# Performance work log

Hardware: AMD Instinct MI355X
Metric: run time of the kernel (lower is better)

## Reference

```python
import jax, jax.numpy as jnp
import numpy as np

C_S, C_Z, C_H = 384, 128, 32
N, L = 4, 384
EPS = 1e-5  # torch LayerNorm default


def setup_inputs() -> dict:
    key = jax.random.key(0)
    ks = jax.random.split(key, 8)
    s = jax.random.normal(ks[0], (N, L, C_S), dtype=jnp.float32)
    ln_g = jnp.ones((C_S,), jnp.float32)
    ln_b = jnp.zeros((C_S,), jnp.float32)
    W1 = jax.random.normal(ks[1], (C_S, C_H), jnp.float32) / np.sqrt(C_S)
    b1 = jax.random.normal(ks[2], (C_H,), jnp.float32) * 0.02
    W2 = jax.random.normal(ks[3], (C_S, C_H), jnp.float32) / np.sqrt(C_S)
    b2 = jax.random.normal(ks[4], (C_H,), jnp.float32) * 0.02
    # linear_out has init='final' (zeros) in training; use random values for a
    # meaningful numerical baseline.
    Wo = jax.random.normal(ks[5], (C_H * C_H, C_Z), jnp.float32) / np.sqrt(C_H * C_H)
    bo = jax.random.normal(ks[6], (C_Z,), jnp.float32) * 0.02
    return {"s": s, "ln_g": ln_g, "ln_b": ln_b, "W1": W1, "b1": b1,
            "W2": W2, "b2": b2, "Wo": Wo, "bo": bo}


def reference(s, ln_g, ln_b, W1, b1, W2, b2, Wo, bo):
    # LayerNorm over c_s
    mu = jnp.mean(s, axis=-1, keepdims=True)
    var = jnp.mean(jnp.square(s - mu), axis=-1, keepdims=True)
    sn = (s - mu) * jax.lax.rsqrt(var + EPS) * ln_g + ln_b
    a = sn @ W1 + b1  # [N, L, c_h]
    b = sn @ W2 + b2  # [N, L, c_h]
    # Original: outer product a[n,i,c]*b[n,j,d] flattened as c*c_h+d, then linear_out.
    # Algebraically fused: never materialize the [N,L,L,c_h^2] tensor.
    Wo3 = Wo.reshape(C_H, C_H, C_Z)  # index order (c, d, z) matches c*c_h+d flattening
    z = jnp.einsum('nic,njd,cdz->nijz', a, b, Wo3, optimize=True) + bo
    return z  # [N, L, L, c_z]
```

## Files before the change

### kernel.cpp

```cpp
#include <hip/hip_runtime.h>
#include <hip/hip_bf16.h>

#define CS 384
#define CH 32
#define CZ 128
#define LL 384
#define NL 1536
#define EPS 1e-5f

typedef float v2f __attribute__((ext_vector_type(2)));
typedef float v4f __attribute__((ext_vector_type(4)));
typedef short s8v __attribute__((ext_vector_type(8)));
typedef unsigned short u8s __attribute__((ext_vector_type(8)));

static __device__ __forceinline__ unsigned short f2bf(float x) {
    unsigned int b = __float_as_uint(x);
    b += 0x7FFFu + ((b >> 16) & 1u);
    return (unsigned short)(b >> 16);
}

__global__ __launch_bounds__(128) void k_ln_ab(
    const float* __restrict__ s, const float* __restrict__ g, const float* __restrict__ be,
    const float* __restrict__ W1, const float* __restrict__ b1,
    const float* __restrict__ W2, const float* __restrict__ b2,
    float* __restrict__ A, float* __restrict__ B)
{
    const int row = blockIdx.x;
    const int t   = threadIdx.x;
    const int wid = t >> 6, lane = t & 63;
    const float* srow = s + (size_t)row * CS;

    __shared__ float sn[CS];
    __shared__ float red[2];
    __shared__ float part[128];

    float x0 = srow[t], x1 = srow[t + 128], x2 = srow[t + 256];

    float p = x0 + x1 + x2;
    #pragma unroll
    for (int o = 32; o > 0; o >>= 1) p += __shfl_down(p, o);
    if (lane == 0) red[wid] = p;
    __syncthreads();
    const float mu = (red[0] + red[1]) * (1.0f / CS);
    __syncthreads();

    float d0 = x0 - mu, d1 = x1 - mu, d2 = x2 - mu;
    float q = d0 * d0 + d1 * d1 + d2 * d2;
    #pragma unroll
    for (int o = 32; o > 0; o >>= 1) q += __shfl_down(q, o);
    if (lane == 0) red[wid] = q;
    __syncthreads();
    const float var = (red[0] + red[1]) * (1.0f / CS);
    const float rstd = rsqrtf(var + EPS);

    sn[t]       = d0 * rstd * g[t]       + be[t];
    sn[t + 128] = d1 * rstd * g[t + 128] + be[t + 128];
    sn[t + 256] = d2 * rstd * g[t + 256] + be[t + 256];
    __syncthreads();

    {
        const int h    = t & 31;
        const int mat  = (t >> 5) & 1;
        const int half = t >> 6;
        const float* W = mat ? W2 : W1;
        float acc = 0.0f;
        const int c0 = half * (CS / 2);
        #pragma unroll 8
        for (int c = c0; c < c0 + CS / 2; ++c)
            acc += sn[c] * W[c * CH + h];
        part[t] = acc;
    }
    __syncthreads();
    if (t < 64) {
        const int h   = t & 31;
        const int mat = t >> 5;
        const float v = part[t] + part[t + 64] + (mat ? b2[h] : b1[h]);
        (mat ? B : A)[(size_t)row * CH + h] = v;
    }
}

__global__ __launch_bounds__(64) void k_packB(
    const float* __restrict__ B, unsigned short* __restrict__ Bf)
{
    const int jt = blockIdx.x;
    const int n  = blockIdx.y;
    const int l  = threadIdx.x;
    const int row = jt * 16 + (l & 15);
    const int g   = l >> 4;
    const float* src = B + ((size_t)(n * LL + row)) * CH + g * 8;
    u8s o;
    #pragma unroll
    for (int e = 0; e < 8; ++e) o[e] = f2bf(src[e]);
    *(u8s*)(Bf + (((size_t)(n * 24 + jt)) * 64 + l) * 8) = o;
}

__global__ __launch_bounds__(256, 2) void k_m2(
    const float* __restrict__ A, const float* __restrict__ Wo,
    unsigned short* __restrict__ Mf)
{
    const int t  = threadIdx.x;
    const int r0 = blockIdx.x * 4;
    __shared__ float Al[4][CH];
    __shared__ float Msub[4 * 32 * 128];
    if (t < 128) Al[t >> 5][t & 31] = A[(size_t)(r0 + (t >> 5)) * CH + (t & 31)];
    __syncthreads();

    const v4f* Wo4 = (const v4f*)Wo;

    #pragma unroll
    for (int it = 0; it < 4; ++it) {
        const int col = t + it * 256;
        v4f acc[4];
        #pragma unroll
        for (int r = 0; r < 4; ++r) acc[r] = (v4f)(0.f);
        #pragma unroll 8
        for (int c = 0; c < CH; ++c) {
            const v4f wv = Wo4[(size_t)c * 1024 + col];
            #pragma unroll
            for (int r = 0; r < 4; ++r)
                acc[r] += Al[r][c] * wv;
        }
        #pragma unroll
        for (int r = 0; r < 4; ++r)
            *((v4f*)&Msub[r * 4096 + col * 4]) = acc[r];
    }
    __syncthreads();

    #pragma unroll
    for (int i = 0; i < 8; ++i) {
        const int item = t + i * 256;
        const int l  = item & 63;
        const int zt = (item >> 6) & 7;
        const int rr = item >> 9;
        const int g  = l >> 4;
        const int z  = zt * 16 + (l & 15);
        u8s o;
        #pragma unroll
        for (int e = 0; e < 8; ++e)
            o[e] = f2bf(Msub[rr * 4096 + (g * 8 + e) * 128 + z]);
        *(u8s*)(Mf + (((size_t)(r0 + rr) * 8 + zt) * 64 + l) * 8) = o;
    }
}

__global__ __launch_bounds__(256, 4) void k_out(
    const unsigned short* __restrict__ Bf, const unsigned short* __restrict__ Mf,
    const float* __restrict__ bo, float* __restrict__ out)
{
    const int r = blockIdx.x;
    const int t = threadIdx.x;
    const int l = t & 63, w = t >> 6;
    const int g = l >> 4, c16 = l & 15;
    const int n = r / LL;

    s8v mf[8];
    {
        const s8v* Mfr = (const s8v*)(Mf + (size_t)r * 8 * 64 * 8);
        #pragma unroll
        for (int zt = 0; zt < 8; ++zt) mf[zt] = Mfr[zt * 64 + l];
    }
    v4f bov[8];
    #pragma unroll
    for (int zt = 0; zt < 8; ++zt) bov[zt] = *(const v4f*)(bo + zt * 16 + g * 4);

    const s8v* Bfn = (const s8v*)(Bf + (size_t)n * 24 * 64 * 8);
    v4f* outv = (v4f*)(out + (size_t)r * LL * CZ);

    for (int jt = w; jt < 24; jt += 4) {
        const s8v af = Bfn[jt * 64 + l];
        v4f* p = outv + (size_t)(jt * 16 + c16) * 32 + g;
        #pragma unroll
        for (int zt = 0; zt < 8; ++zt) {
            v4f d = __builtin_amdgcn_mfma_f32_16x16x32_bf16(mf[zt], af, (v4f)(0.f), 0, 0, 0);
            p[zt * 4] = d + bov[zt];
        }
    }
}

extern "C" void kernel_launch(void* const* d_in, const int* in_sizes, int n_in,
                              void* d_out, int out_size, void* d_ws, size_t ws_size,
                              hipStream_t stream) {
    const float* s  = (const float*)d_in[0];
    const float* g  = (const float*)d_in[1];
    const float* be = (const float*)d_in[2];
    const float* W1 = (const float*)d_in[3];
    const float* b1 = (const float*)d_in[4];
    const float* W2 = (const float*)d_in[5];
    const float* b2 = (const float*)d_in[6];
    const float* Wo = (const float*)d_in[7];
    const float* bo = (const float*)d_in[8];
    float* out = (float*)d_out;

    if (ws_size < 491520u + 12582912u) return;
    float* A  = (float*)d_ws;
    float* Bm = A + (size_t)NL * CH;
    unsigned short* Bf = (unsigned short*)((char*)d_ws + 393216);
    unsigned short* Mf = (unsigned short*)((char*)d_ws + 491520);

    k_ln_ab<<<NL, 128, 0, stream>>>(s, g, be, W1, b1, W2, b2, A, Bm);
    dim3 gpb(24, 4);
    k_packB<<<gpb, 64, 0, stream>>>(Bm, Bf);
    k_m2  <<<NL / 4, 256, 0, stream>>>(A, Wo, Mf);
    k_out <<<NL, 256, 0, stream>>>(Bf, Mf, bo, out);
}
```

Baseline: 95.73 us.

## Fuse layernorm, projections, B packing and M precompute into one prep kernel

```diff
diff --git a/kernel.cpp b/kernel.cpp
--- a/kernel.cpp
+++ b/kernel.cpp
@@ -8,7 +8,6 @@
 #define NL 1536
 #define EPS 1e-5f
 
-typedef float v2f __attribute__((ext_vector_type(2)));
 typedef float v4f __attribute__((ext_vector_type(4)));
 typedef short s8v __attribute__((ext_vector_type(8)));
 typedef unsigned short u8s __attribute__((ext_vector_type(8)));
@@ -19,126 +18,109 @@
     return (unsigned short)(b >> 16);
 }
 
-__global__ __launch_bounds__(128) void k_ln_ab(
+__global__ __launch_bounds__(256, 1) void k_prep(
     const float* __restrict__ s, const float* __restrict__ g, const float* __restrict__ be,
-    const float* __restrict__ W1, const float* __restrict__ b1,
-    const float* __restrict__ W2, const float* __restrict__ b2,
-    float* __restrict__ A, float* __restrict__ B)
+    const float* __restrict__ W1, const float* __restrict__ pb1,
+    const float* __restrict__ W2, const float* __restrict__ pb2,
+    const float* __restrict__ Wo,
+    unsigned short* __restrict__ Bf, unsigned short* __restrict__ Mf)
 {
-    const int row = blockIdx.x;
+    const int blk = blockIdx.x;
+    const int r0  = blk * 16;
+    const int n   = blk / 24;
+    const int jt  = blk % 24;
     const int t   = threadIdx.x;
-    const int wid = t >> 6, lane = t & 63;
-    const float* srow = s + (size_t)row * CS;
 
-    __shared__ float sn[CS];
-    __shared__ float red[2];
-    __shared__ float part[128];
+    __shared__ float Afl[16][32];
+    __shared__ float Bfl[16][32];
+    __shared__ __align__(16) float big[8192];
 
-    float x0 = srow[t], x1 = srow[t + 128], x2 = srow[t + 256];
-
-    float p = x0 + x1 + x2;
-    #pragma unroll
-    for (int o = 32; o > 0; o >>= 1) p += __shfl_down(p, o);
-    if (lane == 0) red[wid] = p;
-    __syncthreads();
-    const float mu = (red[0] + red[1]) * (1.0f / CS);
-    __syncthreads();
-
-    float d0 = x0 - mu, d1 = x1 - mu, d2 = x2 - mu;
-    float q = d0 * d0 + d1 * d1 + d2 * d2;
-    #pragma unroll
-    for (int o = 32; o > 0; o >>= 1) q += __shfl_down(q, o);
-    if (lane == 0) red[wid] = q;
-    __syncthreads();
-    const float var = (red[0] + red[1]) * (1.0f / CS);
-    const float rstd = rsqrtf(var + EPS);
-
-    sn[t]       = d0 * rstd * g[t]       + be[t];
-    sn[t + 128] = d1 * rstd * g[t + 128] + be[t + 128];
-    sn[t + 256] = d2 * rstd * g[t + 256] + be[t + 256];
+    {
+        const int row = t >> 4, l16 = t & 15;
+        const float* srow = s + (size_t)(r0 + row) * CS;
+        float x[24];
+        #pragma unroll
+        for (int k = 0; k < 24; ++k) x[k] = srow[l16 + k * 16];
+        float p = 0.f;
+        #pragma unroll
+        for (int k = 0; k < 24; ++k) p += x[k];
+        #pragma unroll
+        for (int m = 1; m < 16; m <<= 1) p += __shfl_xor(p, m);
+        const float mu = p * (1.0f / CS);
+        float q = 0.f;
+        #pragma unroll
+        for (int k = 0; k < 24; ++k) { float d = x[k] - mu; q += d * d; }
+        #pragma unroll
+        for (int m = 1; m < 16; m <<= 1) q += __shfl_xor(q, m);
+        const float rstd = rsqrtf(q * (1.0f / CS) + EPS);
+        #pragma unroll
+        for (int k = 0; k < 24; ++k) {
+            const int c = l16 + k * 16;
+            big[row * 388 + c] = (x[k] - mu) * rstd * g[c] + be[c];
+        }
+    }
     __syncthreads();
 
     {
-        const int h    = t & 31;
-        const int mat  = (t >> 5) & 1;
-        const int half = t >> 6;
-        const float* W = mat ? W2 : W1;
-        float acc = 0.0f;
-        const int c0 = half * (CS / 2);
-        #pragma unroll 8
-        for (int c = c0; c < c0 + CS / 2; ++c)
-            acc += sn[c] * W[c * CH + h];
-        part[t] = acc;
-    }
-    __syncthreads();
-    if (t < 64) {
-        const int h   = t & 31;
-        const int mat = t >> 5;
-        const float v = part[t] + part[t + 64] + (mat ? b2[h] : b1[h]);
-        (mat ? B : A)[(size_t)row * CH + h] = v;
-    }
-}
-
-__global__ __launch_bounds__(64) void k_packB(
-    const float* __restrict__ B, unsigned short* __restrict__ Bf)
-{
-    const int jt = blockIdx.x;
-    const int n  = blockIdx.y;
-    const int l  = threadIdx.x;
-    const int row = jt * 16 + (l & 15);
-    const int g   = l >> 4;
-    const float* src = B + ((size_t)(n * LL + row)) * CH + g * 8;
-    u8s o;
-    #pragma unroll
-    for (int e = 0; e < 8; ++e) o[e] = f2bf(src[e]);
-    *(u8s*)(Bf + (((size_t)(n * 24 + jt)) * 64 + l) * 8) = o;
-}
-
-__global__ __launch_bounds__(256, 2) void k_m2(
-    const float* __restrict__ A, const float* __restrict__ Wo,
-    unsigned short* __restrict__ Mf)
-{
-    const int t  = threadIdx.x;
-    const int r0 = blockIdx.x * 4;
-    __shared__ float Al[4][CH];
-    __shared__ float Msub[4 * 32 * 128];
-    if (t < 128) Al[t >> 5][t & 31] = A[(size_t)(r0 + (t >> 5)) * CH + (t & 31)];
-    __syncthreads();
-
-    const v4f* Wo4 = (const v4f*)Wo;
-
-    #pragma unroll
-    for (int it = 0; it < 4; ++it) {
-        const int col = t + it * 256;
-        v4f acc[4];
-        #pragma unroll
-        for (int r = 0; r < 4; ++r) acc[r] = (v4f)(0.f);
-        #pragma unroll 8
-        for (int c = 0; c < CH; ++c) {
-            const v4f wv = Wo4[(size_t)c * 1024 + col];
-            #pragma unroll
-            for (int r = 0; r < 4; ++r)
-                acc[r] += Al[r][c] * wv;
+        const int h = t & 31, rg = t >> 5;
+        const float* sn0 = big + (rg * 2) * 388;
+        const float* sn1 = sn0 + 388;
+        float a0 = 0.f, a1 = 0.f, c0 = 0.f, c1 = 0.f;
+        #pragma unroll 4
+        for (int c = 0; c < CS; ++c) {
+            const float w1 = W1[c * CH + h];
+            const float w2 = W2[c * CH + h];
+            const float s0 = sn0[c], s1 = sn1[c];
+            a0 += s0 * w1; a1 += s1 * w1;
+            c0 += s0 * w2; c1 += s1 * w2;
         }
-        #pragma unroll
-        for (int r = 0; r < 4; ++r)
-            *((v4f*)&Msub[r * 4096 + col * 4]) = acc[r];
+        Afl[rg * 2][h]     = a0 + pb1[h];
+        Afl[rg * 2 + 1][h] = a1 + pb1[h];
+        Bfl[rg * 2][h]     = c0 + pb2[h];
+        Bfl[rg * 2 + 1][h] = c1 + pb2[h];
     }
     __syncthreads();
 
-    #pragma unroll
-    for (int i = 0; i < 8; ++i) {
-        const int item = t + i * 256;
-        const int l  = item & 63;
-        const int zt = (item >> 6) & 7;
-        const int rr = item >> 9;
-        const int g  = l >> 4;
-        const int z  = zt * 16 + (l & 15);
+    if (t < 64) {
+        const int row16 = t & 15, gq = t >> 4;
         u8s o;
         #pragma unroll
-        for (int e = 0; e < 8; ++e)
-            o[e] = f2bf(Msub[rr * 4096 + (g * 8 + e) * 128 + z]);
-        *(u8s*)(Mf + (((size_t)(r0 + rr) * 8 + zt) * 64 + l) * 8) = o;
+        for (int e = 0; e < 8; ++e) o[e] = f2bf(Bfl[row16][gq * 8 + e]);
+        *(u8s*)(Bf + (((size_t)(n * 24 + jt)) * 64 + t) * 8) = o;
+    }
+
+    const int zq = t & 31, dd = t >> 5;
+    for (int ch = 0; ch < 4; ++ch) {
+        for (int rh = 0; rh < 2; ++rh) {
+            __syncthreads();
+            v4f acc[8];
+            #pragma unroll
+            for (int rr = 0; rr < 8; ++rr) acc[rr] = (v4f)(0.f);
+            const float* wop = Wo + (ch * 8 + dd) * 128 + zq * 4;
+            #pragma unroll 4
+            for (int c = 0; c < CH; ++c) {
+                const v4f wv = *(const v4f*)(wop + (size_t)c * 4096);
+                #pragma unroll
+                for (int rr = 0; rr < 8; ++rr)
+                    acc[rr] += Afl[rh * 8 + rr][c] * wv;
+            }
+            #pragma unroll
+            for (int rr = 0; rr < 8; ++rr)
+                *(v4f*)(big + rr * 1024 + dd * 128 + zq * 4) = acc[rr];
+            __syncthreads();
+            #pragma unroll
+            for (int i = 0; i < 4; ++i) {
+                const int item = t + i * 256;
+                const int c16 = item & 15;
+                const int zt  = (item >> 4) & 7;
+                const int rr  = item >> 7;
+                u8s o;
+                #pragma unroll
+                for (int e = 0; e < 8; ++e)
+                    o[e] = f2bf(big[rr * 1024 + e * 128 + zt * 16 + c16]);
+                *(u8s*)(Mf + (((size_t)(r0 + rh * 8 + rr) * 8 + zt) * 64 + ch * 16 + c16) * 8) = o;
+            }
+        }
     }
 }
 
@@ -190,15 +172,10 @@
     const float* bo = (const float*)d_in[8];
     float* out = (float*)d_out;
 
-    if (ws_size < 491520u + 12582912u) return;
-    float* A  = (float*)d_ws;
-    float* Bm = A + (size_t)NL * CH;
-    unsigned short* Bf = (unsigned short*)((char*)d_ws + 393216);
-    unsigned short* Mf = (unsigned short*)((char*)d_ws + 491520);
+    if (ws_size < 98304u + 12582912u) return;
+    unsigned short* Bf = (unsigned short*)d_ws;
+    unsigned short* Mf = (unsigned short*)((char*)d_ws + 98304);
 
-    k_ln_ab<<<NL, 128, 0, stream>>>(s, g, be, W1, b1, W2, b2, A, Bm);
-    dim3 gpb(24, 4);
-    k_packB<<<gpb, 64, 0, stream>>>(Bm, Bf);
-    k_m2  <<<NL / 4, 256, 0, stream>>>(A, Wo, Mf);
+    k_prep<<<96, 256, 0, stream>>>(s, g, be, W1, b1, W2, b2, Wo, Bf, Mf);
     k_out <<<NL, 256, 0, stream>>>(Bf, Mf, bo, out);
 }
```

New measurement: 121.3 us. +26.7%, slower.
